# Performance work log

Measured on AMD Instinct MI355X. Metric: run time of the kernel, lower is better.

## Reference

```python
import jax, jax.numpy as jnp
import numpy as np

D_MODEL = 1024
ATT_MODEL = 1024
NHEAD = 16
HEAD_DIM = ATT_MODEL // NHEAD
B, S = 2, 2048


def setup_inputs() -> dict:
    key = jax.random.key(0)
    ks = jax.random.split(key, 5)
    sc = 1.0 / np.sqrt(D_MODEL)
    return {
        "x": jax.random.normal(ks[0], (B, S, D_MODEL), dtype=jnp.float32),
        "Wq": jax.random.normal(ks[1], (D_MODEL, ATT_MODEL), dtype=jnp.float32) * sc,
        "bq": jnp.zeros((ATT_MODEL,), dtype=jnp.float32),
        "Wk": jax.random.normal(ks[2], (D_MODEL, ATT_MODEL), dtype=jnp.float32) * sc,
        "bk": jnp.zeros((ATT_MODEL,), dtype=jnp.float32),
        "Wv": jax.random.normal(ks[3], (D_MODEL, ATT_MODEL), dtype=jnp.float32) * sc,
        "bv": jnp.zeros((ATT_MODEL,), dtype=jnp.float32),
        "Wo": jax.random.normal(ks[4], (ATT_MODEL, D_MODEL), dtype=jnp.float32) * sc,
        "bo": jnp.zeros((D_MODEL,), dtype=jnp.float32),
    }


def reference(x, Wq, bq, Wk, bk, Wv, bv, Wo, bo):
    b, s, _ = x.shape
    # projections [B,S,att_model] -> [B,H,S,Dh]
    def split_heads(t):
        return t.reshape(b, s, NHEAD, HEAD_DIM).transpose(0, 2, 1, 3)
    Q = split_heads(x @ Wq + bq)
    K = split_heads(x @ Wk + bk)
    V = split_heads(x @ Wv + bv)
    # dk = sqrt(att_model / nhead) = sqrt(head_dim)
    dk = jnp.asarray(HEAD_DIM, x.dtype) ** 0.5
    scores = jnp.einsum("bhqd,bhkd->bhqk", Q, K) / dk  # [B,H,S,S]
    attn = jax.nn.softmax(scores, axis=-1)
    out = jnp.einsum("bhqk,bhkd->bhqd", attn, V)       # [B,H,S,Dh]
    out = out.transpose(0, 2, 1, 3).reshape(b, s, ATT_MODEL)
    return out @ Wo + bo
```

## Files before the change

kernel.cpp:

```cpp
#include <hip/hip_runtime.h>
#include <hip/hip_bf16.h>
#include <math.h>

#define D_MODEL 1024
#define ATT 1024
#define NHEAD 16
#define HDIM 64
#define BATCH 2
#define SEQ 2048
#define M_ROWS (BATCH * SEQ)

typedef unsigned short u16;
typedef unsigned int u32;
typedef __bf16 bf16x8 __attribute__((ext_vector_type(8)));
typedef float f4 __attribute__((ext_vector_type(4)));
typedef u16 u16x8 __attribute__((ext_vector_type(8)));
typedef u16 u16x4 __attribute__((ext_vector_type(4)));

static_assert(sizeof(u16x8) == 16, "u16x8 must be 16B");

__device__ __forceinline__ u16 f32_to_bf16(float f) {
    union { float f; unsigned u; } c; c.f = f;
    unsigned u = c.u;
    return (u16)((u + 0x7FFFu + ((u >> 16) & 1u)) >> 16);
}
__device__ __forceinline__ float bf16_to_f32(u16 h) {
    union { unsigned u; float f; } c; c.u = ((unsigned)h) << 16;
    return c.f;
}
__device__ __forceinline__ void split2(float f, u16& hi, u16& lo) {
    hi = f32_to_bf16(f);
    lo = f32_to_bf16(f - bf16_to_f32(hi));
}

__device__ __forceinline__ f4 mfma16(u16x8 a, u16x8 b, f4 c) {
    union U { u16x8 u; bf16x8 b; };
    U ua, ub; ua.u = a; ub.u = b;
    return __builtin_amdgcn_mfma_f32_16x16x32_bf16(ua.b, ub.b, c, 0, 0, 0);
}

__device__ __forceinline__ void gload16(const void* g, void* l) {
    __builtin_amdgcn_global_load_lds(
        (const __attribute__((address_space(1))) void*)g,
        (__attribute__((address_space(3))) void*)l, 16, 0, 0);
}

template <int N>
__device__ __forceinline__ void waitcnt_vm() {
    if constexpr (N == 0)      asm volatile("s_waitcnt vmcnt(0)" ::: "memory");
    else if constexpr (N == 4) asm volatile("s_waitcnt vmcnt(4)" ::: "memory");
    else if constexpr (N == 6) asm volatile("s_waitcnt vmcnt(6)" ::: "memory");
    else if constexpr (N == 8) asm volatile("s_waitcnt vmcnt(8)" ::: "memory");
}
#define BARRIER() __builtin_amdgcn_s_barrier()

__global__ __launch_bounds__(256) void k_split(const float* __restrict__ in,
                                               u16* __restrict__ hi,
                                               u16* __restrict__ lo, int n4) {
    int i = blockIdx.x * blockDim.x + threadIdx.x;
    if (i >= n4) return;
    const float4 v = ((const float4*)in)[i];
    float vv[4] = {v.x, v.y, v.z, v.w};
    u16 hh[4], ll[4];
#pragma unroll
    for (int j = 0; j < 4; ++j) split2(vv[j], hh[j], ll[j]);
    u16x4 hv = {hh[0], hh[1], hh[2], hh[3]};
    u16x4 lv = {ll[0], ll[1], ll[2], ll[3]};
    *(u16x4*)(hi + (size_t)i * 4) = hv;
    *(u16x4*)(lo + (size_t)i * 4) = lv;
}

__global__ __launch_bounds__(256) void k_splitT(const float* __restrict__ W,
                                                u16* __restrict__ hiT,
                                                u16* __restrict__ loT) {
    __shared__ float tile[32][33];
    int n0 = blockIdx.x * 32, k0 = blockIdx.y * 32;
    int tx = threadIdx.x, ty = threadIdx.y;
#pragma unroll
    for (int j = 0; j < 4; ++j) {
        int r = ty + j * 8;
        tile[r][tx] = W[(size_t)(k0 + r) * ATT + n0 + tx];
    }
    __syncthreads();
#pragma unroll
    for (int j = 0; j < 4; ++j) {
        int r = ty + j * 8;
        float v = tile[tx][r];
        u16 h, l; split2(v, h, l);
        hiT[(size_t)(n0 + r) * D_MODEL + k0 + tx] = h;
        loT[(size_t)(n0 + r) * D_MODEL + k0 + tx] = l;
    }
}

__global__ __launch_bounds__(256) void k_transpose(
    const u16* __restrict__ src_h, const u16* __restrict__ src_l,
    u16* __restrict__ dst_h, u16* __restrict__ dst_l, int srcld, int dstld) {
    __shared__ u16 t[64][72];
    const u16* src = blockIdx.z ? src_l : src_h;
    u16* dst = blockIdx.z ? dst_l : dst_h;
    int n0 = blockIdx.x * 64, m0 = blockIdx.y * 64;
    int tid = threadIdx.x;
    int r = tid >> 2, c16 = (tid & 3) * 16;
    *(u16x8*)&t[r][c16]     = *(const u16x8*)&src[(size_t)(m0 + r) * srcld + n0 + c16];
    *(u16x8*)&t[r][c16 + 8] = *(const u16x8*)&src[(size_t)(m0 + r) * srcld + n0 + c16 + 8];
    __syncthreads();
    u16x8 o0, o1;
#pragma unroll
    for (int j = 0; j < 8; ++j) { o0[j] = t[c16 + j][r]; o1[j] = t[c16 + 8 + j][r]; }
    *(u16x8*)&dst[(size_t)(n0 + r) * dstld + m0 + c16]     = o0;
    *(u16x8*)&dst[(size_t)(n0 + r) * dstld + m0 + c16 + 8] = o1;
}

template <int MF, int SPLIT_OUT>
__global__ __launch_bounds__(256) void k_gemm(
    const u16* __restrict__ Ah, const u16* __restrict__ Al,
    const u16* __restrict__ Bh, const u16* __restrict__ Bl,
    const float* __restrict__ bq, const float* __restrict__ bk,
    const float* __restrict__ bv,
    float* __restrict__ Co, u16* __restrict__ Ch, u16* __restrict__ Cl,
    int M, int N, int K, int NBX) {
    constexpr int BM = MF * 32;
    constexpr int SAe = BM * 32;
    constexpr int NCH = (2 * BM + 256) / 16;
    constexpr int CPW = NCH / 4;
    constexpr int BUFE = (2 * BM + 256) * 32;
    __shared__ u16 sh[2 * BUFE];

    int tid = threadIdx.x;
    int wave = tid >> 6, lane = tid & 63, lg = lane >> 4, ln = lane & 15;
    int wm = wave >> 1, wn = wave & 1;

    int nb = gridDim.x;
    int bs = (blockIdx.x & 7) * (nb >> 3) + (blockIdx.x >> 3);
    int bx = bs % NBX, by = bs / NBX;
    int m0 = by * BM, n0 = bx * 128;

    f4 acc[MF][4];
#pragma unroll
    for (int i = 0; i < MF; ++i)
#pragma unroll
        for (int j = 0; j < 4; ++j) acc[i][j] = f4{0.f, 0.f, 0.f, 0.f};

    const u16* gp[CPW];
#pragma unroll
    for (int j = 0; j < CPW; ++j) {
        int c = wave * CPW + j;
        int bo = c << 10;
        const u16* base; int local, r0;
        if (bo < BM * 64)                { base = Ah; local = bo;                 r0 = m0; }
        else if (bo < 2 * BM * 64)       { base = Al; local = bo - BM * 64;       r0 = m0; }
        else if (bo < 2 * BM * 64 + 8192){ base = Bh; local = bo - 2 * BM * 64;   r0 = n0; }
        else                             { base = Bl; local = bo - 2 * BM * 64 - 8192; r0 = n0; }
        int lo2 = local + lane * 16;
        int row = lo2 >> 6;
        int cb  = (lo2 >> 4) & 3;
        int cbs = cb ^ ((row >> 1) & 3);
        gp[j] = base + (size_t)(r0 + row) * K + cbs * 8;
    }

    int offA[MF], offB[4];
#pragma unroll
    for (int mf = 0; mf < MF; ++mf) {
        int row = wm * (MF * 16) + mf * 16 + ln;
        offA[mf] = row * 32 + ((lg ^ ((row >> 1) & 3)) << 3);
    }
#pragma unroll
    for (int nf = 0; nf < 4; ++nf) {
        int row = wn * 64 + nf * 16 + ln;
        offB[nf] = row * 32 + ((lg ^ ((row >> 1) & 3)) << 3);
    }

    auto stage = [&](int bsel) {
#pragma unroll
        for (int j = 0; j < CPW; ++j)
            gload16(gp[j], (char*)sh + bsel * (BUFE * 2) + ((wave * CPW + j) << 10));
    };
    auto adv = [&]() {
#pragma unroll
        for (int j = 0; j < CPW; ++j) gp[j] += 32;
    };
    auto compute = [&](int sb) {
        u16x8 a_h[MF], a_l[MF], b_h[4], b_l[4];
#pragma unroll
        for (int mf = 0; mf < MF; ++mf) {
            a_h[mf] = *(const u16x8*)&sh[sb + offA[mf]];
            a_l[mf] = *(const u16x8*)&sh[sb + SAe + offA[mf]];
        }
#pragma unroll
        for (int nf = 0; nf < 4; ++nf) {
            b_h[nf] = *(const u16x8*)&sh[sb + 2 * SAe + offB[nf]];
            b_l[nf] = *(const u16x8*)&sh[sb + 2 * SAe + 4096 + offB[nf]];
        }
#pragma unroll
        for (int mf = 0; mf < MF; ++mf)
#pragma unroll
            for (int nf = 0; nf < 4; ++nf) {
                acc[mf][nf] = mfma16(a_h[mf], b_h[nf], acc[mf][nf]);
                acc[mf][nf] = mfma16(a_h[mf], b_l[nf], acc[mf][nf]);
                acc[mf][nf] = mfma16(a_l[mf], b_h[nf], acc[mf][nf]);
            }
    };

    const int NS = K / 32;
    stage(0); adv();
    for (int t = 0; t < NS - 2; t += 2) {
        stage(1); adv();
        waitcnt_vm<CPW>(); BARRIER();
        compute(0);
        BARRIER();
        stage(0); adv();
        waitcnt_vm<CPW>(); BARRIER();
        compute(BUFE);
        BARRIER();
    }
    stage(1);
    waitcnt_vm<CPW>(); BARRIER();
    compute(0);
    BARRIER();
    waitcnt_vm<0>(); BARRIER();
    compute(BUFE);

#pragma unroll
    for (int mf = 0; mf < MF; ++mf)
#pragma unroll
        for (int nf = 0; nf < 4; ++nf) {
            int col = n0 + wn * 64 + nf * 16 + ln;
            float bb;
            if (bk) bb = col < 1024 ? bq[col] : (col < 2048 ? bk[col - 1024] : bv[col - 2048]);
            else    bb = bq[col];
#pragma unroll
            for (int r = 0; r < 4; ++r) {
                int row = m0 + wm * (MF * 16) + mf * 16 + lg * 4 + r;
                float v = acc[mf][nf][r] + bb;
                if (SPLIT_OUT) {
                    u16 h, l; split2(v, h, l);
                    Ch[(size_t)row * N + col] = h;
                    if (col < 1024) Cl[(size_t)row * N + col] = l;
                } else {
                    Co[(size_t)row * N + col] = v;
                }
            }
        }
}

#define ATTN_SCALE 0.18033688f

__global__ __launch_bounds__(256) void k_attn(
    const u16* __restrict__ qkv_h, const u16* __restrict__ qkv_l,
    const u16* __restrict__ vt,
    u16* __restrict__ Oh, u16* __restrict__ Ol) {
    __shared__ u16 sh[24576];
    int tid = threadIdx.x;
    int w = tid >> 6, lane = tid & 63, lg = lane >> 4, ln = lane & 15;

    int bs = (blockIdx.x & 7) * 64 + (blockIdx.x >> 3);
    int qt = bs & 15, h = (bs >> 4) & 15, b = bs >> 8;
    int q0 = qt * 128;

    u16x8 qh[2][2], ql[2][2];
#pragma unroll
    for (int mf = 0; mf < 2; ++mf) {
        int row = q0 + w * 32 + mf * 16 + ln;
        const u16* ph_ = qkv_h + (size_t)(b * SEQ + row) * 3072 + h * HDIM;
        const u16* pl_ = qkv_l + (size_t)(b * SEQ + row) * 3072 + h * HDIM;
#pragma unroll
        for (int ks = 0; ks < 2; ++ks) {
            qh[mf][ks] = *(const u16x8*)(ph_ + ks * 32 + lg * 8);
            ql[mf][ks] = *(const u16x8*)(pl_ + ks * 32 + lg * 8);
        }
    }

    f4 acco[2][4], accl[2];
#pragma unroll
    for (int i = 0; i < 2; ++i) {
#pragma unroll
        for (int j = 0; j < 4; ++j) acco[i][j] = f4{0.f, 0.f, 0.f, 0.f};
        accl[i] = f4{0.f, 0.f, 0.f, 0.f};
    }
    float run_m[2][4];
#pragma unroll
    for (int i = 0; i < 2; ++i)
#pragma unroll
        for (int r = 0; r < 4; ++r) run_m[i][r] = -INFINITY;

    u16x8 ones;
#pragma unroll
    for (int j = 0; j < 8; ++j) ones[j] = 0x3F80;

    int bt = w >> 1, hf = w & 1;
    const u16* gp[4];
    {
        int r0 = hf * 32 + (lane >> 3);
        int kbs = (lane & 7) ^ (lane >> 3);
        if (bt == 0) {
            const u16* base = qkv_h + (size_t)(b * SEQ) * 3072 + 1024 + h * HDIM;
#pragma unroll
            for (int j = 0; j < 4; ++j)
                gp[j] = base + (size_t)(r0 + j * 8) * 3072 + kbs * 8;
        } else {
            const u16* base = vt + (size_t)(h * HDIM) * M_ROWS + b * SEQ;
#pragma unroll
            for (int j = 0; j < 4; ++j)
                gp[j] = base + (size_t)(r0 + j * 8) * M_ROWS + kbs * 8;
        }
    }
    const int gstride = (bt == 0) ? 64 * 3072 : 64;
    const int cb0 = (w * 4) << 10;

    auto stage = [&](int bsel) {
#pragma unroll
        for (int j = 0; j < 4; ++j)
            gload16(gp[j], (char*)sh + cb0 + (j << 10) + bsel * 16384);
    };
    auto adv = [&]() {
#pragma unroll
        for (int j = 0; j < 4; ++j) gp[j] += gstride;
    };

    int offQK[4][2], offPr[2][2];
#pragma unroll
    for (int nf = 0; nf < 4; ++nf) {
        int krow = nf * 16 + ln;
#pragma unroll
        for (int ks = 0; ks < 2; ++ks)
            offQK[nf][ks] = krow * 64 + (((4 * ks + lg) ^ (krow & 7)) << 3);
    }
#pragma unroll
    for (int mf = 0; mf < 2; ++mf) {
        int prow = w * 32 + mf * 16 + ln;
#pragma unroll
        for (int ks = 0; ks < 2; ++ks)
            offPr[mf][ks] = 16384 + prow * 64 + (((4 * ks + lg) ^ (prow & 7)) << 3);
    }

    auto compute = [&](int base) {
        f4 s[2][4];
#pragma unroll
        for (int i = 0; i < 2; ++i)
#pragma unroll
            for (int j = 0; j < 4; ++j) s[i][j] = f4{0.f, 0.f, 0.f, 0.f};
#pragma unroll
        for (int nf = 0; nf < 4; ++nf) {
#pragma unroll
            for (int ks = 0; ks < 2; ++ks) {
                u16x8 bh = *(const u16x8*)&sh[base + offQK[nf][ks]];
#pragma unroll
                for (int mf = 0; mf < 2; ++mf) {
                    s[mf][nf] = mfma16(qh[mf][ks], bh, s[mf][nf]);
                    s[mf][nf] = mfma16(ql[mf][ks], bh, s[mf][nf]);
                }
            }
        }
#pragma unroll
        for (int mf = 0; mf < 2; ++mf) {
#pragma unroll
            for (int r = 0; r < 4; ++r) {
                float mx = fmaxf(fmaxf(s[mf][0][r], s[mf][1][r]),
                                 fmaxf(s[mf][2][r], s[mf][3][r]));
#pragma unroll
                for (int d = 1; d < 16; d <<= 1) mx = fmaxf(mx, __shfl_xor(mx, d));
                float mx2 = mx * ATTN_SCALE;
                bool need = mx2 > run_m[mf][r] + 11.0f;
                float nm = need ? mx2 : run_m[mf][r];
                int qrow = w * 32 + mf * 16 + lg * 4 + r;
                int swz = qrow & 7;
                int pbase = 16384 + qrow * 64 + (ln & 7);
#pragma unroll
                for (int nf = 0; nf < 4; ++nf) {
                    float p = __builtin_amdgcn_exp2f(s[mf][nf][r] * ATTN_SCALE - nm);
                    sh[pbase + (((nf * 2 + (ln >> 3)) ^ swz) << 3)] = f32_to_bf16(p);
                }
                if (__any((int)need)) {
                    float corr = __builtin_amdgcn_exp2f(run_m[mf][r] - nm);
#pragma unroll
                    for (int nf = 0; nf < 4; ++nf) acco[mf][nf][r] *= corr;
                    accl[mf][r] *= corr;
                    run_m[mf][r] = nm;
                }
            }
        }
#pragma unroll
        for (int ks = 0; ks < 2; ++ks) {
            u16x8 pa[2];
#pragma unroll
            for (int mf = 0; mf < 2; ++mf)
                pa[mf] = *(const u16x8*)&sh[offPr[mf][ks]];
#pragma unroll
            for (int nf = 0; nf < 4; ++nf) {
                u16x8 vh = *(const u16x8*)&sh[base + 4096 + offQK[nf][ks]];
#pragma unroll
                for (int mf = 0; mf < 2; ++mf)
                    acco[mf][nf] = mfma16(pa[mf], vh, acco[mf][nf]);
            }
            accl[0] = mfma16(pa[0], ones, accl[0]);
            accl[1] = mfma16(pa[1], ones, accl[1]);
        }
    };

    stage(0); adv();
    for (int t = 0; t < 30; t += 2) {
        stage(1); adv();
        waitcnt_vm<4>(); BARRIER();
        compute(0);
        BARRIER();
        stage(0); adv();
        waitcnt_vm<4>(); BARRIER();
        compute(8192);
        BARRIER();
    }
    stage(1);
    waitcnt_vm<4>(); BARRIER();
    compute(0);
    BARRIER();
    waitcnt_vm<0>(); BARRIER();
    compute(8192);

#pragma unroll
    for (int mf = 0; mf < 2; ++mf)
#pragma unroll
        for (int nf = 0; nf < 4; ++nf) {
            int col = h * HDIM + nf * 16 + ln;
#pragma unroll
            for (int r = 0; r < 4; ++r) {
                int row = q0 + w * 32 + mf * 16 + lg * 4 + r;
                float v = acco[mf][nf][r] / accl[mf][r];
                u16 hh, ll; split2(v, hh, ll);
                Oh[(size_t)(b * SEQ + row) * ATT + col] = hh;
                Ol[(size_t)(b * SEQ + row) * ATT + col] = ll;
            }
        }
}

extern "C" void kernel_launch(void* const* d_in, const int* in_sizes, int n_in,
                              void* d_out, int out_size, void* d_ws, size_t ws_size,
                              hipStream_t stream) {
    const float* x  = (const float*)d_in[0];
    const float* Wq = (const float*)d_in[1];
    const float* bq = (const float*)d_in[2];
    const float* Wk = (const float*)d_in[3];
    const float* bk = (const float*)d_in[4];
    const float* Wv = (const float*)d_in[5];
    const float* bv = (const float*)d_in[6];
    const float* Wo = (const float*)d_in[7];
    const float* bo = (const float*)d_in[8];
    float* out = (float*)d_out;

    const size_t MK = (size_t)M_ROWS * ATT;
    const size_t WE = (size_t)D_MODEL * ATT;
    const size_t M3 = (size_t)M_ROWS * 3072;

    char* p = (char*)d_ws;
    auto alloc = [&](size_t bytes) -> u16* {
        u16* r = (u16*)p;
        p += (bytes + 255) & ~(size_t)255;
        return r;
    };
    u16* x_hi  = alloc(MK * 2); u16* x_lo  = alloc(MK * 2);
    u16* wT_h  = alloc(3 * WE * 2); u16* wT_l  = alloc(3 * WE * 2);
    u16* woT_h = alloc(WE * 2); u16* woT_l = alloc(WE * 2);
    u16* qkv_h = alloc(M3 * 2); u16* qkv_l = alloc(M3 * 2);
    u16* vt_h  = alloc(MK * 2); u16* vt_l  = alloc(MK * 2);
    u16* at_h = x_hi; u16* at_l = x_lo;

    k_split<<<dim3((unsigned)(MK / 4 / 256)), 256, 0, stream>>>(x, x_hi, x_lo, (int)(MK / 4));

    dim3 bt(32, 8), gt(32, 32);
    k_splitT<<<gt, bt, 0, stream>>>(Wq, wT_h, wT_l);
    k_splitT<<<gt, bt, 0, stream>>>(Wk, wT_h + WE, wT_l + WE);
    k_splitT<<<gt, bt, 0, stream>>>(Wv, wT_h + 2 * WE, wT_l + 2 * WE);
    k_splitT<<<gt, bt, 0, stream>>>(Wo, woT_h, woT_l);

    k_gemm<4, 1><<<768, 256, 0, stream>>>(x_hi, x_lo, wT_h, wT_l, bq, bk, bv,
                                          nullptr, qkv_h, qkv_l, M_ROWS, 3072, 1024, 24);

    k_transpose<<<dim3(16, 64, 1), 256, 0, stream>>>(qkv_h + 2048, qkv_l + 2048,
                                                     vt_h, vt_l, 3072, M_ROWS);

    k_attn<<<512, 256, 0, stream>>>(qkv_h, qkv_l, vt_h, at_h, at_l);

    k_gemm<2, 0><<<512, 256, 0, stream>>>(at_h, at_l, woT_h, woT_l, bo, nullptr, nullptr,
                                          out, nullptr, nullptr, M_ROWS, 1024, 1024, 8);
}
```

Before: 315.0 us.

## Use fp16 QKV and attention MFMAs instead of split bf16 hi/lo

The QKV projection now writes a single fp16 output instead of bf16 hi/lo pairs. Attention runs QK^T and PV with fp16 MFMAs, which halves the QK MFMA count and drops the low-part Q loads and stores. The online-softmax rescale is restructured so the cross-lane max reduction only runs when some lane might exceed the threshold. This trades the extra precision of the split representation for fp16 precision and range, which risks overflow or accuracy loss on other inputs.

```diff
diff --git a/kernel.cpp b/kernel.cpp
--- a/kernel.cpp
+++ b/kernel.cpp
@@ -13,6 +13,7 @@
 typedef unsigned short u16;
 typedef unsigned int u32;
 typedef __bf16 bf16x8 __attribute__((ext_vector_type(8)));
+typedef _Float16 f16x8 __attribute__((ext_vector_type(8)));
 typedef float f4 __attribute__((ext_vector_type(4)));
 typedef u16 u16x8 __attribute__((ext_vector_type(8)));
 typedef u16 u16x4 __attribute__((ext_vector_type(4)));
@@ -32,11 +33,19 @@
     hi = f32_to_bf16(f);
     lo = f32_to_bf16(f - bf16_to_f32(hi));
 }
+__device__ __forceinline__ u16 f32_to_f16bits(float f) {
+    union { _Float16 h; u16 u; } c; c.h = (_Float16)f; return c.u;
+}
 
 __device__ __forceinline__ f4 mfma16(u16x8 a, u16x8 b, f4 c) {
     union U { u16x8 u; bf16x8 b; };
     U ua, ub; ua.u = a; ub.u = b;
     return __builtin_amdgcn_mfma_f32_16x16x32_bf16(ua.b, ub.b, c, 0, 0, 0);
+}
+__device__ __forceinline__ f4 mfma16h(u16x8 a, u16x8 b, f4 c) {
+    union U { u16x8 u; f16x8 h; };
+    U ua, ub; ua.u = a; ub.u = b;
+    return __builtin_amdgcn_mfma_f32_16x16x32_f16(ua.h, ub.h, c, 0, 0, 0);
 }
 
 __device__ __forceinline__ void gload16(const void* g, void* l) {
@@ -93,11 +102,8 @@
 }
 
 __global__ __launch_bounds__(256) void k_transpose(
-    const u16* __restrict__ src_h, const u16* __restrict__ src_l,
-    u16* __restrict__ dst_h, u16* __restrict__ dst_l, int srcld, int dstld) {
+    const u16* __restrict__ src, u16* __restrict__ dst, int srcld, int dstld) {
     __shared__ u16 t[64][72];
-    const u16* src = blockIdx.z ? src_l : src_h;
-    u16* dst = blockIdx.z ? dst_l : dst_h;
     int n0 = blockIdx.x * 64, m0 = blockIdx.y * 64;
     int tid = threadIdx.x;
     int r = tid >> 2, c16 = (tid & 3) * 16;
@@ -117,7 +123,7 @@
     const u16* __restrict__ Bh, const u16* __restrict__ Bl,
     const float* __restrict__ bq, const float* __restrict__ bk,
     const float* __restrict__ bv,
-    float* __restrict__ Co, u16* __restrict__ Ch, u16* __restrict__ Cl,
+    float* __restrict__ Co, u16* __restrict__ Ch,
     int M, int N, int K, int NBX) {
     constexpr int BM = MF * 32;
     constexpr int SAe = BM * 32;
@@ -233,9 +239,7 @@
                 int row = m0 + wm * (MF * 16) + mf * 16 + lg * 4 + r;
                 float v = acc[mf][nf][r] + bb;
                 if (SPLIT_OUT) {
-                    u16 h, l; split2(v, h, l);
-                    Ch[(size_t)row * N + col] = h;
-                    if (col < 1024) Cl[(size_t)row * N + col] = l;
+                    Ch[(size_t)row * N + col] = f32_to_f16bits(v);
                 } else {
                     Co[(size_t)row * N + col] = v;
                 }
@@ -246,8 +250,7 @@
 #define ATTN_SCALE 0.18033688f
 
 __global__ __launch_bounds__(256) void k_attn(
-    const u16* __restrict__ qkv_h, const u16* __restrict__ qkv_l,
-    const u16* __restrict__ vt,
+    const u16* __restrict__ qkv, const u16* __restrict__ vt,
     u16* __restrict__ Oh, u16* __restrict__ Ol) {
     __shared__ u16 sh[24576];
     int tid = threadIdx.x;
@@ -257,17 +260,14 @@
     int qt = bs & 15, h = (bs >> 4) & 15, b = bs >> 8;
     int q0 = qt * 128;
 
-    u16x8 qh[2][2], ql[2][2];
+    u16x8 qh[2][2];
 #pragma unroll
     for (int mf = 0; mf < 2; ++mf) {
         int row = q0 + w * 32 + mf * 16 + ln;
-        const u16* ph_ = qkv_h + (size_t)(b * SEQ + row) * 3072 + h * HDIM;
-        const u16* pl_ = qkv_l + (size_t)(b * SEQ + row) * 3072 + h * HDIM;
-#pragma unroll
-        for (int ks = 0; ks < 2; ++ks) {
+        const u16* ph_ = qkv + (size_t)(b * SEQ + row) * 3072 + h * HDIM;
+#pragma unroll
+        for (int ks = 0; ks < 2; ++ks)
             qh[mf][ks] = *(const u16x8*)(ph_ + ks * 32 + lg * 8);
-            ql[mf][ks] = *(const u16x8*)(pl_ + ks * 32 + lg * 8);
-        }
     }
 
     f4 acco[2][4], accl[2];
@@ -285,7 +285,7 @@
 
     u16x8 ones;
 #pragma unroll
-    for (int j = 0; j < 8; ++j) ones[j] = 0x3F80;
+    for (int j = 0; j < 8; ++j) ones[j] = 0x3C00;
 
     int bt = w >> 1, hf = w & 1;
     const u16* gp[4];
@@ -293,7 +293,7 @@
         int r0 = hf * 32 + (lane >> 3);
         int kbs = (lane & 7) ^ (lane >> 3);
         if (bt == 0) {
-            const u16* base = qkv_h + (size_t)(b * SEQ) * 3072 + 1024 + h * HDIM;
+            const u16* base = qkv + (size_t)(b * SEQ) * 3072 + 1024 + h * HDIM;
 #pragma unroll
             for (int j = 0; j < 4; ++j)
                 gp[j] = base + (size_t)(r0 + j * 8) * 3072 + kbs * 8;
@@ -345,38 +345,36 @@
             for (int ks = 0; ks < 2; ++ks) {
                 u16x8 bh = *(const u16x8*)&sh[base + offQK[nf][ks]];
 #pragma unroll
-                for (int mf = 0; mf < 2; ++mf) {
-                    s[mf][nf] = mfma16(qh[mf][ks], bh, s[mf][nf]);
-                    s[mf][nf] = mfma16(ql[mf][ks], bh, s[mf][nf]);
-                }
+                for (int mf = 0; mf < 2; ++mf)
+                    s[mf][nf] = mfma16h(qh[mf][ks], bh, s[mf][nf]);
             }
         }
 #pragma unroll
         for (int mf = 0; mf < 2; ++mf) {
 #pragma unroll
             for (int r = 0; r < 4; ++r) {
-                float mx = fmaxf(fmaxf(s[mf][0][r], s[mf][1][r]),
-                                 fmaxf(s[mf][2][r], s[mf][3][r]));
-#pragma unroll
-                for (int d = 1; d < 16; d <<= 1) mx = fmaxf(mx, __shfl_xor(mx, d));
-                float mx2 = mx * ATTN_SCALE;
-                bool need = mx2 > run_m[mf][r] + 11.0f;
-                float nm = need ? mx2 : run_m[mf][r];
-                int qrow = w * 32 + mf * 16 + lg * 4 + r;
-                int swz = qrow & 7;
-                int pbase = 16384 + qrow * 64 + (ln & 7);
-#pragma unroll
-                for (int nf = 0; nf < 4; ++nf) {
-                    float p = __builtin_amdgcn_exp2f(s[mf][nf][r] * ATTN_SCALE - nm);
-                    sh[pbase + (((nf * 2 + (ln >> 3)) ^ swz) << 3)] = f32_to_bf16(p);
-                }
-                if (__any((int)need)) {
+                float lmx = fmaxf(fmaxf(s[mf][0][r], s[mf][1][r]),
+                                  fmaxf(s[mf][2][r], s[mf][3][r]));
+                bool maybe = lmx * ATTN_SCALE > run_m[mf][r] + 11.0f;
+                if (__any((int)maybe)) {
+                    float mx = lmx;
+#pragma unroll
+                    for (int d = 1; d < 16; d <<= 1) mx = fmaxf(mx, __shfl_xor(mx, d));
+                    float nm = fmaxf(run_m[mf][r], mx * ATTN_SCALE);
                     float corr = __builtin_amdgcn_exp2f(run_m[mf][r] - nm);
 #pragma unroll
                     for (int nf = 0; nf < 4; ++nf) acco[mf][nf][r] *= corr;
                     accl[mf][r] *= corr;
                     run_m[mf][r] = nm;
                 }
+                int qrow = w * 32 + mf * 16 + lg * 4 + r;
+                int swz = qrow & 7;
+                int pbase = 16384 + qrow * 64 + (ln & 7);
+#pragma unroll
+                for (int nf = 0; nf < 4; ++nf) {
+                    float p = __builtin_amdgcn_exp2f(s[mf][nf][r] * ATTN_SCALE - run_m[mf][r]);
+                    sh[pbase + (((nf * 2 + (ln >> 3)) ^ swz) << 3)] = f32_to_f16bits(p);
+                }
             }
         }
 #pragma unroll
@@ -390,10 +388,10 @@
                 u16x8 vh = *(const u16x8*)&sh[base + 4096 + offQK[nf][ks]];
 #pragma unroll
                 for (int mf = 0; mf < 2; ++mf)
-                    acco[mf][nf] = mfma16(pa[mf], vh, acco[mf][nf]);
-            }
-            accl[0] = mfma16(pa[0], ones, accl[0]);
-            accl[1] = mfma16(pa[1], ones, accl[1]);
+                    acco[mf][nf] = mfma16h(pa[mf], vh, acco[mf][nf]);
+            }
+            accl[0] = mfma16h(pa[0], ones, accl[0]);
+            accl[1] = mfma16h(pa[1], ones, accl[1]);
         }
     };
 
@@ -458,8 +456,8 @@
     u16* x_hi  = alloc(MK * 2); u16* x_lo  = alloc(MK * 2);
     u16* wT_h  = alloc(3 * WE * 2); u16* wT_l  = alloc(3 * WE * 2);
     u16* woT_h = alloc(WE * 2); u16* woT_l = alloc(WE * 2);
-    u16* qkv_h = alloc(M3 * 2); u16* qkv_l = alloc(M3 * 2);
-    u16* vt_h  = alloc(MK * 2); u16* vt_l  = alloc(MK * 2);
+    u16* qkv   = alloc(M3 * 2);
+    u16* vt    = alloc(MK * 2);
     u16* at_h = x_hi; u16* at_l = x_lo;
 
     k_split<<<dim3((unsigned)(MK / 4 / 256)), 256, 0, stream>>>(x, x_hi, x_lo, (int)(MK / 4));
@@ -471,13 +469,12 @@
     k_splitT<<<gt, bt, 0, stream>>>(Wo, woT_h, woT_l);
 
     k_gemm<4, 1><<<768, 256, 0, stream>>>(x_hi, x_lo, wT_h, wT_l, bq, bk, bv,
-                                          nullptr, qkv_h, qkv_l, M_ROWS, 3072, 1024, 24);
-
-    k_transpose<<<dim3(16, 64, 1), 256, 0, stream>>>(qkv_h + 2048, qkv_l + 2048,
-                                                     vt_h, vt_l, 3072, M_ROWS);
-
-    k_attn<<<512, 256, 0, stream>>>(qkv_h, qkv_l, vt_h, at_h, at_l);
+                                          nullptr, qkv, M_ROWS, 3072, 1024, 24);
+
+    k_transpose<<<dim3(16, 64), 256, 0, stream>>>(qkv + 2048, vt, 3072, M_ROWS);
+
+    k_attn<<<512, 256, 0, stream>>>(qkv, vt, at_h, at_l);
 
     k_gemm<2, 0><<<512, 256, 0, stream>>>(at_h, at_l, woT_h, woT_l, bo, nullptr, nullptr,
-                                          out, nullptr, nullptr, M_ROWS, 1024, 1024, 8);
-}
+                                          out, nullptr, M_ROWS, 1024, 1024, 8);
+}
```

Result: faster. 277.4 us (-11.9%).
